# Kernel optimization log

Hardware: AMD Instinct MI355X
Metric: run time of the kernel (lower is better)

Reference implementation:

```python
import jax, jax.numpy as jnp
import numpy as np

EPS = 1e-5
NEG_SLOPE = 0.01

def layer_norm(x, w, b):
    m = jnp.mean(x, axis=-1, keepdims=True)
    v = jnp.var(x, axis=-1, keepdims=True)
    return (x - m) / jnp.sqrt(v + EPS) * w + b

def _lin_init(key, out_dim, in_dim):
    s = 1.0 / np.sqrt(in_dim)
    k1, k2 = jax.random.split(key)
    W = jax.random.uniform(k1, (out_dim, in_dim), jnp.float32, -s, s)
    b = jax.random.uniform(k2, (out_dim,), jnp.float32, -s, s)
    return W, b

def setup_inputs() -> dict:
    key = jax.random.key(0)
    ks = jax.random.split(key, 12)
    N_S = 100000; N_T = 100000; E = 2000000; H1 = 64; H2 = 32
    x_s = jax.random.normal(ks[0], (N_S, 2), jnp.float32)
    x_t = jax.random.normal(ks[1], (N_T, 2), jnp.float32)
    edge_index = jax.random.randint(ks[2], (2, E), 0, N_S, jnp.int32)
    edge_attr = jax.random.uniform(ks[3], (E,), jnp.float32)
    w0, b0 = _lin_init(ks[4], H1, 3)
    w1, b1 = _lin_init(ks[5], H1, H1)
    w2, b2 = _lin_init(ks[6], H1, H1)
    w3, b3 = _lin_init(ks[7], 1, H1)
    ln_w = jnp.ones((3, H1), jnp.float32)
    ln_b = jnp.zeros((3, H1), jnp.float32)
    fw1, fb1 = _lin_init(ks[8], H2, 4)
    fln_w = jnp.ones((H2,), jnp.float32)
    fln_b = jnp.zeros((H2,), jnp.float32)
    fw2, fb2 = _lin_init(ks[9], 1, H2)
    return dict(x_s=x_s, x_t=x_t, edge_index=edge_index, edge_attr=edge_attr,
                w0=w0, b0=b0, w1=w1, b1=b1, w2=w2, b2=b2, w3=w3, b3=b3,
                ln_w=ln_w, ln_b=ln_b, fw1=fw1, fb1=fb1, fln_w=fln_w, fln_b=fln_b,
                fw2=fw2, fb2=fb2)

def reference(x_s, x_t, edge_index, edge_attr, w0, b0, w1, b1, w2, b2, w3, b3,
              ln_w, ln_b, fw1, fb1, fln_w, fln_b, fw2, fb2):
    src = edge_index[0]
    dst = edge_index[1]
    x_s_d = x_s[src, 1][:, None]           # [E,1]
    x_s_c = x_t[dst, 1][:, None]           # [E,1]
    y = jnp.concatenate([x_s_d, x_s_c, edge_attr[:, None]], axis=1)  # [E,3]
    # MLP chain: Linear -> LeakyReLU -> (dropout eval: identity) -> LayerNorm
    for i, (W, b) in enumerate([(w0, b0), (w1, b1), (w2, b2)]):
        y = layer_norm(jax.nn.leaky_relu(y @ W.T + b, NEG_SLOPE), ln_w[i], ln_b[i])
    y = jax.nn.relu(y @ w3.T + b3)[:, 0]   # [E]
    # index_add scatter then re-gather
    y_sum_i = jax.ops.segment_sum(y, src, num_segments=x_s.shape[0])[src][:, None]
    y_sum_j = jax.ops.segment_sum(y, dst, num_segments=x_t.shape[0])[dst][:, None]
    coef = jnp.concatenate([x_s_d, y_sum_i, x_s_c, y_sum_j], axis=1)  # [E,4]
    coef = layer_norm(jax.nn.relu(coef @ fw1.T + fb1), fln_w, fln_b)
    coef = jax.nn.relu(coef @ fw2.T + fb2)[:, 0]
    return y * coef
```

## Files before the change

kernel.cpp:

```cpp
#include <hip/hip_runtime.h>

#define H2 32

#define SIG_F32  0x3F800000u
#define SIG_BF16 0x3F803F80u

typedef float v4f __attribute__((ext_vector_type(4)));
typedef short s8v __attribute__((ext_vector_type(8)));
typedef unsigned u4v __attribute__((ext_vector_type(4)));

__global__ void zero_f(float* __restrict__ p, int n) {
    int i = blockIdx.x * blockDim.x + threadIdx.x;
    if (i < n) p[i] = 0.0f;
}

template<bool BF16>
__device__ __forceinline__ float LD(const void* p, int i) {
    if (BF16) {
        unsigned int u = ((unsigned int)((const unsigned short*)p)[i]) << 16;
        return __uint_as_float(u);
    }
    return ((const float*)p)[i];
}

template<bool BF16>
__device__ __forceinline__ void ST(void* p, int i, float v) {
    if (BF16) {
        unsigned int u = __float_as_uint(v);
        unsigned int r = (u + 0x7FFFu + ((u >> 16) & 1u)) >> 16;
        ((unsigned short*)p)[i] = (unsigned short)r;
    } else {
        ((float*)p)[i] = v;
    }
}

__device__ __forceinline__ unsigned short bf16_rne(float x) {
    unsigned int u = __float_as_uint(x);
    return (unsigned short)((u + 0x7FFFu + ((u >> 16) & 1u)) >> 16);
}

__device__ __forceinline__ void split2(float x0, float x1,
                                       unsigned& hw, unsigned& lw) {
    unsigned h;
    asm("v_cvt_pk_bf16_f32 %0, %1, %2" : "=v"(h) : "v"(x0), "v"(x1));
    const float h0 = __uint_as_float(h << 16);
    const float h1 = __uint_as_float(h & 0xFFFF0000u);
    unsigned l;
    asm("v_cvt_pk_bf16_f32 %0, %1, %2" : "=v"(l) : "v"(x0 - h0), "v"(x1 - h1));
    hw = h; lw = l;
}

__device__ __align__(16) unsigned short g_A[2 * 2 * 4 * 2 * 512];
__device__ __align__(16) float g_S[2][64], g_C[2][64];
__device__ __align__(16) float g_l0[64 * 4];
__device__ __align__(16) float g_w3g[64];
__device__ float g_sc3[2];

template<bool BF16>
__device__ __forceinline__ void fold_body(
    const void* w0, const void* b0, const void* w1, const void* b1,
    const void* w2, const void* b2, const void* w3, const void* b3,
    const void* lnw, const void* lnb) {
    const int b = blockIdx.x;
    const int k = threadIdx.x;
    if (b < 128) {
        const int L = b >> 6, j = b & 63;
        const void* w  = L ? w2 : w1;
        const void* bb = L ? b2 : b1;
        const float wv = LD<BF16>(w, j * 64 + k);
        const float wt = wv * LD<BF16>(lnw, L * 64 + k);
        float s = wt;
        float c = wv * LD<BF16>(lnb, L * 64 + k);
        #pragma unroll
        for (int off = 1; off < 64; off <<= 1) {
            s += __shfl_xor(s, off);
            c += __shfl_xor(c, off);
        }
        if (k == 0) {
            g_S[L][j] = s;
            g_C[L][j] = c + LD<BF16>(bb, j);
        }
    } else {
        const int j = k;
        g_l0[4 * j + 0] = LD<BF16>(w0, 3 * j);
        g_l0[4 * j + 1] = LD<BF16>(w0, 3 * j + 1);
        g_l0[4 * j + 2] = LD<BF16>(w0, 3 * j + 2);
        g_l0[4 * j + 3] = LD<BF16>(b0, j);
        const float w3g = LD<BF16>(w3, j) * LD<BF16>(lnw, 128 + j);
        g_w3g[j] = w3g;
        float S = w3g;
        float C = LD<BF16>(w3, j) * LD<BF16>(lnb, 128 + j);
        #pragma unroll
        for (int off = 1; off < 64; off <<= 1) {
            S += __shfl_xor(S, off);
            C += __shfl_xor(C, off);
        }
        if (j == 0) { g_sc3[0] = S; g_sc3[1] = C + LD<BF16>(b3, 0); }
    }
}

__global__ void setup_fold(const void* __restrict__ w0, const void* __restrict__ b0,
                           const void* __restrict__ w1, const void* __restrict__ b1,
                           const void* __restrict__ w2, const void* __restrict__ b2,
                           const void* __restrict__ w3, const void* __restrict__ b3,
                           const void* __restrict__ lnw, const void* __restrict__ lnb) {
    const unsigned int sig = *(const unsigned int*)lnw;
    if (sig == SIG_BF16)
        fold_body<true>(w0, b0, w1, b1, w2, b2, w3, b3, lnw, lnb);
    else
        fold_body<false>(w0, b0, w1, b1, w2, b2, w3, b3, lnw, lnb);
}

template<bool BF16>
__device__ __forceinline__ void frag_body(const void* w1, const void* w2,
                                          const void* lnw) {
    const int b  = blockIdx.x;
    const int L  = b >> 3, jt = (b >> 1) & 3, ks = b & 1;
    const int l  = threadIdx.x, m = l & 15, g = l >> 4;
    const void* w = L ? w2 : w1;
    const int row = 16 * jt + m;
    const int blkH = ((L * 2 + 0) * 4 + jt) * 2 + ks;
    const int blkL = ((L * 2 + 1) * 4 + jt) * 2 + ks;
    #pragma unroll
    for (int i = 0; i < 8; ++i) {
        const int k = 32 * ks + 8 * g + i;
        const float x = LD<BF16>(w, row * 64 + k) * LD<BF16>(lnw, L * 64 + k);
        const unsigned short hi = bf16_rne(x);
        const float hif = __uint_as_float(((unsigned int)hi) << 16);
        const unsigned short lo = bf16_rne(x - hif);
        g_A[blkH * 512 + l * 8 + i] = hi;
        g_A[blkL * 512 + l * 8 + i] = lo;
    }
}

__global__ void setup_frag(const void* __restrict__ w1, const void* __restrict__ w2,
                           const void* __restrict__ lnw) {
    const unsigned int sig = *(const unsigned int*)lnw;
    if (sig == SIG_BF16) frag_body<true>(w1, w2, lnw);
    else                 frag_body<false>(w1, w2, lnw);
}

template<bool BF16>
__device__ __forceinline__ void edge_body(
    const void* xs, const void* xt, const int* ei, const void* ea,
    void* ystage, float* ssrc, float* sdst, int E, unsigned char* Hb) {

    const int tid = threadIdx.x;
    const int l   = tid & 63;
    const int wid = __builtin_amdgcn_readfirstlane(tid >> 6);
    unsigned char* Hw = Hb + wid * 8192;
    const int m16 = l & 15, g = l >> 4;

    const int tile = blockIdx.x * 4 + wid;
    const int e0 = tile * 32;
    if (e0 >= E) return;

    int srcA[2], dstA[2];
    float av[2], cv[2], wv[2];
    #pragma unroll
    for (int s = 0; s < 2; ++s) {
        int e = e0 + s * 16 + m16;
        int ec = e < E ? e : 0;
        srcA[s] = ei[ec]; dstA[s] = ei[E + ec];
        av[s] = LD<BF16>(xs, 2 * srcA[s] + 1);
        cv[s] = LD<BF16>(xt, 2 * dstA[s] + 1);
        wv[s] = LD<BF16>(ea, ec);
    }

    float m_[2], r_[2];

    s8v Bh[2][2], Bl[2][2];
    {
        float ps[2] = {0.f, 0.f}, ps2[2] = {0.f, 0.f};
        #pragma unroll
        for (int s = 0; s < 2; ++s) {
            #pragma unroll
            for (int ks = 0; ks < 2; ++ks) {
                u4v th, tl;
                #pragma unroll
                for (int q = 0; q < 4; ++q) {
                    const int f = 32 * ks + 8 * g + 2 * q;
                    const v4f qa = *(const v4f*)&g_l0[4 * f];
                    const v4f qb = *(const v4f*)&g_l0[4 * (f + 1)];
                    float x0 = qa.w + av[s] * qa.x + cv[s] * qa.y + wv[s] * qa.z;
                    float x1 = qb.w + av[s] * qb.x + cv[s] * qb.y + wv[s] * qb.z;
                    x0 = fmaxf(x0, 0.01f * x0);
                    x1 = fmaxf(x1, 0.01f * x1);
                    ps[s] += x0 + x1; ps2[s] += x0 * x0 + x1 * x1;
                    unsigned hw, lw;
                    split2(x0, x1, hw, lw);
                    th[q] = hw; tl[q] = lw;
                }
                Bh[s][ks] = __builtin_bit_cast(s8v, th);
                Bl[s][ks] = __builtin_bit_cast(s8v, tl);
            }
            float a0 = ps[s], a1 = ps2[s];
            a0 += __shfl_xor(a0, 16); a0 += __shfl_xor(a0, 32);
            a1 += __shfl_xor(a1, 16); a1 += __shfl_xor(a1, 32);
            m_[s] = a0 * (1.f / 64.f);
            r_[s] = rsqrtf(a1 * (1.f / 64.f) - m_[s] * m_[s] + 1e-5f);
        }
    }

    {
        float psA[2] = {0.f, 0.f}, ps2A[2] = {0.f, 0.f};
        #pragma unroll
        for (int jt = 0; jt < 4; ++jt) {
            const s8v Ah0 = *(const s8v*)(g_A + ((0 + jt) * 2 + 0) * 512 + l * 8);
            const s8v Ah1 = *(const s8v*)(g_A + ((0 + jt) * 2 + 1) * 512 + l * 8);
            const s8v Al0 = *(const s8v*)(g_A + ((4 + jt) * 2 + 0) * 512 + l * 8);
            const s8v Al1 = *(const s8v*)(g_A + ((4 + jt) * 2 + 1) * 512 + l * 8);
            const v4f Sv = *(const v4f*)&g_S[0][16 * jt + 4 * g];
            const v4f Cv = *(const v4f*)&g_C[0][16 * jt + 4 * g];
            #pragma unroll
            for (int s = 0; s < 2; ++s) {
                v4f a0 = {0.f, 0.f, 0.f, 0.f};
                v4f a1 = {0.f, 0.f, 0.f, 0.f};
                a0 = __builtin_amdgcn_mfma_f32_16x16x32_bf16(Ah0, Bh[s][0], a0, 0, 0, 0);
                a1 = __builtin_amdgcn_mfma_f32_16x16x32_bf16(Al0, Bh[s][0], a1, 0, 0, 0);
                a0 = __builtin_amdgcn_mfma_f32_16x16x32_bf16(Ah1, Bh[s][1], a0, 0, 0, 0);
                a1 = __builtin_amdgcn_mfma_f32_16x16x32_bf16(Al1, Bh[s][1], a1, 0, 0, 0);
                a0 = __builtin_amdgcn_mfma_f32_16x16x32_bf16(Ah0, Bl[s][0], a0, 0, 0, 0);
                a1 = __builtin_amdgcn_mfma_f32_16x16x32_bf16(Ah1, Bl[s][1], a1, 0, 0, 0);
                float x0 = r_[s] * ((a0[0] + a1[0]) - m_[s] * Sv[0]) + Cv[0];
                float x1 = r_[s] * ((a0[1] + a1[1]) - m_[s] * Sv[1]) + Cv[1];
                float x2 = r_[s] * ((a0[2] + a1[2]) - m_[s] * Sv[2]) + Cv[2];
                float x3 = r_[s] * ((a0[3] + a1[3]) - m_[s] * Sv[3]) + Cv[3];
                x0 = fmaxf(x0, 0.01f * x0); x1 = fmaxf(x1, 0.01f * x1);
                x2 = fmaxf(x2, 0.01f * x2); x3 = fmaxf(x3, 0.01f * x3);
                psA[s]  += x0 + x1 + x2 + x3;
                ps2A[s] += x0 * x0 + x1 * x1 + x2 * x2 + x3 * x3;
                unsigned hw0, lw0, hw1, lw1;
                split2(x0, x1, hw0, lw0);
                split2(x2, x3, hw1, lw1);
                const int el = s * 16 + m16;
                const unsigned sw = (unsigned)((el & 7) << 4);
                const unsigned off = (unsigned)el * 128
                                   + (((unsigned)(32 * jt + 8 * g)) ^ sw);
                uint2 ph; ph.x = hw0; ph.y = hw1;
                uint2 pl; pl.x = lw0; pl.y = lw1;
                *(uint2*)&Hw[off] = ph;
                *(uint2*)&Hw[off + 4096] = pl;
            }
        }
        #pragma unroll
        for (int s = 0; s < 2; ++s) {
            float ps = psA[s], ps2 = ps2A[s];
            ps  += __shfl_xor(ps, 16);  ps  += __shfl_xor(ps, 32);
            ps2 += __shfl_xor(ps2, 16); ps2 += __shfl_xor(ps2, 32);
            m_[s] = ps * (1.f / 64.f);
            r_[s] = rsqrtf(ps2 * (1.f / 64.f) - m_[s] * m_[s] + 1e-5f);
        }
    }

    float pd[2] = {0.f, 0.f};
    {
        #pragma unroll
        for (int s = 0; s < 2; ++s) {
            const int el = s * 16 + m16;
            const unsigned sw = (unsigned)((el & 7) << 4);
            #pragma unroll
            for (int ks = 0; ks < 2; ++ks) {
                const unsigned off = (unsigned)el * 128
                                   + (((unsigned)(16 * g + 64 * ks)) ^ sw);
                Bh[s][ks] = *(const s8v*)&Hw[off];
                Bl[s][ks] = *(const s8v*)&Hw[off + 4096];
            }
        }
        float psA[2] = {0.f, 0.f}, ps2A[2] = {0.f, 0.f};
        #pragma unroll
        for (int jt = 0; jt < 4; ++jt) {
            const s8v Ah0 = *(const s8v*)(g_A + ((8  + jt) * 2 + 0) * 512 + l * 8);
            const s8v Ah1 = *(const s8v*)(g_A + ((8  + jt) * 2 + 1) * 512 + l * 8);
            const s8v Al0 = *(const s8v*)(g_A + ((12 + jt) * 2 + 0) * 512 + l * 8);
            const s8v Al1 = *(const s8v*)(g_A + ((12 + jt) * 2 + 1) * 512 + l * 8);
            const v4f Sv = *(const v4f*)&g_S[1][16 * jt + 4 * g];
            const v4f Cv = *(const v4f*)&g_C[1][16 * jt + 4 * g];
            const v4f w3v = *(const v4f*)&g_w3g[16 * jt + 4 * g];
            #pragma unroll
            for (int s = 0; s < 2; ++s) {
                v4f a0 = {0.f, 0.f, 0.f, 0.f};
                v4f a1 = {0.f, 0.f, 0.f, 0.f};
                a0 = __builtin_amdgcn_mfma_f32_16x16x32_bf16(Ah0, Bh[s][0], a0, 0, 0, 0);
                a1 = __builtin_amdgcn_mfma_f32_16x16x32_bf16(Al0, Bh[s][0], a1, 0, 0, 0);
                a0 = __builtin_amdgcn_mfma_f32_16x16x32_bf16(Ah1, Bh[s][1], a0, 0, 0, 0);
                a1 = __builtin_amdgcn_mfma_f32_16x16x32_bf16(Al1, Bh[s][1], a1, 0, 0, 0);
                a0 = __builtin_amdgcn_mfma_f32_16x16x32_bf16(Ah0, Bl[s][0], a0, 0, 0, 0);
                a1 = __builtin_amdgcn_mfma_f32_16x16x32_bf16(Ah1, Bl[s][1], a1, 0, 0, 0);
                #pragma unroll
                for (int r = 0; r < 4; ++r) {
                    float x = r_[s] * ((a0[r] + a1[r]) - m_[s] * Sv[r]) + Cv[r];
                    x = fmaxf(x, 0.01f * x);
                    psA[s] += x; ps2A[s] += x * x;
                    pd[s] += x * w3v[r];
                }
            }
        }
        #pragma unroll
        for (int s = 0; s < 2; ++s) {
            float ps = psA[s], ps2 = ps2A[s];
            ps  += __shfl_xor(ps, 16);  ps  += __shfl_xor(ps, 32);
            ps2 += __shfl_xor(ps2, 16); ps2 += __shfl_xor(ps2, 32);
            m_[s] = ps * (1.f / 64.f);
            r_[s] = rsqrtf(ps2 * (1.f / 64.f) - m_[s] * m_[s] + 1e-5f);
        }
    }

    #pragma unroll
    for (int s = 0; s < 2; ++s) {
        float d = pd[s];
        d += __shfl_xor(d, 16); d += __shfl_xor(d, 32);
        float t = r_[s] * (d - m_[s] * g_sc3[0]) + g_sc3[1];
        const float yv = fmaxf(t, 0.f);
        if (g == 0) {
            int e = e0 + s * 16 + m16;
            if (e < E) {
                ST<BF16>(ystage, e, yv);
                atomicAdd(&ssrc[srcA[s]], yv);
                atomicAdd(&sdst[dstA[s]], yv);
            }
        }
    }
}

__global__ __launch_bounds__(256, 2)
void edge_mfma(const void* __restrict__ xs, const void* __restrict__ xt,
               const int* __restrict__ ei, const void* __restrict__ ea,
               const void* __restrict__ lnw,
               void* __restrict__ ystage,
               float* __restrict__ ssrc, float* __restrict__ sdst, int E) {
    __shared__ __align__(16) unsigned char lds[4][8192];
    const unsigned int sig = *(const unsigned int*)lnw;
    if (sig == SIG_BF16)
        edge_body<true>(xs, xt, ei, ea, ystage, ssrc, sdst, E, &lds[0][0]);
    else
        edge_body<false>(xs, xt, ei, ea, ystage, ssrc, sdst, E, &lds[0][0]);
}

template<bool BF16>
__device__ __forceinline__ void coef_body(
    const void* xs, const void* xt, const int* ei,
    const void* fw1, const void* fb1, const void* flnw, const void* flnb,
    const void* fw2, const void* fb2,
    const float* ssrc, const float* sdst, void* out, int E) {
    int e = blockIdx.x * blockDim.x + threadIdx.x;
    if (e >= E) return;
    const int src = ei[e], dst = ei[E + e];
    const float c0 = LD<BF16>(xs, 2 * src + 1);
    const float c2 = LD<BF16>(xt, 2 * dst + 1);
    const float c1 = ssrc[src];
    const float c3 = sdst[dst];
    float h[H2];
    float sum = 0.f, sum2 = 0.f;
    #pragma unroll
    for (int j = 0; j < H2; ++j) {
        float t = LD<BF16>(fb1, j) + c0 * LD<BF16>(fw1, 4 * j) + c1 * LD<BF16>(fw1, 4 * j + 1)
                + c2 * LD<BF16>(fw1, 4 * j + 2) + c3 * LD<BF16>(fw1, 4 * j + 3);
        t = (t > 0.f) ? t : 0.f;
        h[j] = t; sum += t; sum2 += t * t;
    }
    const float m = sum * (1.f / H2);
    const float r = rsqrtf(sum2 * (1.f / H2) - m * m + 1e-5f);
    float t = LD<BF16>(fb2, 0);
    #pragma unroll
    for (int j = 0; j < H2; ++j)
        t += ((h[j] - m) * r * LD<BF16>(flnw, j) + LD<BF16>(flnb, j)) * LD<BF16>(fw2, j);
    const float coef = (t > 0.f) ? t : 0.f;
    const float yv = LD<BF16>(out, e);
    ST<BF16>(out, e, yv * coef);
}

__global__ __launch_bounds__(256)
void coef_stage(const void* __restrict__ xs, const void* __restrict__ xt,
                const int* __restrict__ ei,
                const void* __restrict__ fw1, const void* __restrict__ fb1,
                const void* __restrict__ flnw, const void* __restrict__ flnb,
                const void* __restrict__ fw2, const void* __restrict__ fb2,
                const void* __restrict__ lnw,
                const float* __restrict__ ssrc, const float* __restrict__ sdst,
                void* __restrict__ out, int E) {
    const unsigned int sig = *(const unsigned int*)lnw;
    if (sig == SIG_BF16)
        coef_body<true>(xs, xt, ei, fw1, fb1, flnw, flnb, fw2, fb2, ssrc, sdst, out, E);
    else
        coef_body<false>(xs, xt, ei, fw1, fb1, flnw, flnb, fw2, fb2, ssrc, sdst, out, E);
}

extern "C" void kernel_launch(void* const* d_in, const int* in_sizes, int n_in,
                              void* d_out, int out_size, void* d_ws, size_t ws_size,
                              hipStream_t stream) {
    const void* xs = d_in[0];
    const void* xt = d_in[1];
    const int*  ei = (const int*)d_in[2];
    const void* ea = d_in[3];
    const int NS = in_sizes[0] / 2;
    const int NT = in_sizes[1] / 2;
    const int E  = in_sizes[3];

    float* ws   = (float*)d_ws;
    float* ssrc = ws;
    float* sdst = ws + NS;

    const int nz = NS + NT;
    const int gE = (E + 255) / 256;
    zero_f<<<(nz + 255) / 256, 256, 0, stream>>>(ws, nz);

    setup_fold<<<129, 64, 0, stream>>>(
        d_in[4], d_in[5], d_in[6], d_in[7], d_in[8], d_in[9],
        d_in[10], d_in[11], d_in[12], d_in[13]);
    setup_frag<<<16, 64, 0, stream>>>(d_in[6], d_in[8], d_in[12]);

    const int tiles  = (E + 31) / 32;
    const int blocks = (tiles + 3) / 4;
    edge_mfma<<<blocks, 256, 0, stream>>>(
        xs, xt, ei, ea, d_in[12], d_out, ssrc, sdst, E);

    coef_stage<<<gE, 256, 0, stream>>>(
        xs, xt, ei, d_in[14], d_in[15], d_in[16], d_in[17], d_in[18], d_in[19],
        d_in[12], ssrc, sdst, d_out, E);
}
```

Measured before the change: 374.1 us.

## Make edge MFMA kernel persistent with software-prefetched gathers for next tile

The edge kernel becomes a grid-stride persistent loop capped at 1024 blocks. Each wave processes several 32-edge tiles and issues the index and feature gathers for its next tile while the current tile's MFMA layers run, so gather latency is hidden behind compute. The costs are extra live registers for the prefetched data, which may hurt occupancy, and fewer waves in flight to hide latency in other ways.

```diff
diff --git a/kernel.cpp b/kernel.cpp
--- a/kernel.cpp
+++ b/kernel.cpp
@@ -140,6 +140,11 @@
     else                 frag_body<false>(w1, w2, lnw);
 }
 
+struct EdgeData {
+    int   src[2], dst[2];
+    float av[2], cv[2], wv[2];
+};
+
 template<bool BF16>
 __device__ __forceinline__ void edge_body(
     const void* xs, const void* xt, const int* ei, const void* ea,
@@ -151,175 +156,200 @@
     unsigned char* Hw = Hb + wid * 8192;
     const int m16 = l & 15, g = l >> 4;
 
-    const int tile = blockIdx.x * 4 + wid;
-    const int e0 = tile * 32;
-    if (e0 >= E) return;
-
-    int srcA[2], dstA[2];
-    float av[2], cv[2], wv[2];
-    #pragma unroll
-    for (int s = 0; s < 2; ++s) {
-        int e = e0 + s * 16 + m16;
-        int ec = e < E ? e : 0;
-        srcA[s] = ei[ec]; dstA[s] = ei[E + ec];
-        av[s] = LD<BF16>(xs, 2 * srcA[s] + 1);
-        cv[s] = LD<BF16>(xt, 2 * dstA[s] + 1);
-        wv[s] = LD<BF16>(ea, ec);
-    }
-
-    float m_[2], r_[2];
-
-    s8v Bh[2][2], Bl[2][2];
+    const int ntiles = (E + 31) >> 5;
+    const int nwaves = gridDim.x * 4;
+    int t = blockIdx.x * 4 + wid;
+    if (t >= ntiles) return;
+
+    EdgeData ed;
     {
-        float ps[2] = {0.f, 0.f}, ps2[2] = {0.f, 0.f};
+        const int e0 = t << 5;
         #pragma unroll
         for (int s = 0; s < 2; ++s) {
-            #pragma unroll
-            for (int ks = 0; ks < 2; ++ks) {
-                u4v th, tl;
+            int e = e0 + s * 16 + m16;
+            int ec = e < E ? e : 0;
+            ed.src[s] = ei[ec]; ed.dst[s] = ei[E + ec];
+            ed.av[s] = LD<BF16>(xs, 2 * ed.src[s] + 1);
+            ed.cv[s] = LD<BF16>(xt, 2 * ed.dst[s] + 1);
+            ed.wv[s] = LD<BF16>(ea, ec);
+        }
+    }
+
+    for (; t < ntiles; t += nwaves) {
+        const int e0 = t << 5;
+        float m_[2], r_[2];
+        s8v Bh[2][2], Bl[2][2];
+
+        {
+            float ps[2] = {0.f, 0.f}, ps2[2] = {0.f, 0.f};
+            #pragma unroll
+            for (int s = 0; s < 2; ++s) {
                 #pragma unroll
-                for (int q = 0; q < 4; ++q) {
-                    const int f = 32 * ks + 8 * g + 2 * q;
-                    const v4f qa = *(const v4f*)&g_l0[4 * f];
-                    const v4f qb = *(const v4f*)&g_l0[4 * (f + 1)];
-                    float x0 = qa.w + av[s] * qa.x + cv[s] * qa.y + wv[s] * qa.z;
-                    float x1 = qb.w + av[s] * qb.x + cv[s] * qb.y + wv[s] * qb.z;
-                    x0 = fmaxf(x0, 0.01f * x0);
-                    x1 = fmaxf(x1, 0.01f * x1);
-                    ps[s] += x0 + x1; ps2[s] += x0 * x0 + x1 * x1;
-                    unsigned hw, lw;
-                    split2(x0, x1, hw, lw);
-                    th[q] = hw; tl[q] = lw;
+                for (int ks = 0; ks < 2; ++ks) {
+                    u4v th, tl;
+                    #pragma unroll
+                    for (int q = 0; q < 4; ++q) {
+                        const int f = 32 * ks + 8 * g + 2 * q;
+                        const v4f qa = *(const v4f*)&g_l0[4 * f];
+                        const v4f qb = *(const v4f*)&g_l0[4 * (f + 1)];
+                        float x0 = qa.w + ed.av[s] * qa.x + ed.cv[s] * qa.y + ed.wv[s] * qa.z;
+                        float x1 = qb.w + ed.av[s] * qb.x + ed.cv[s] * qb.y + ed.wv[s] * qb.z;
+                        x0 = fmaxf(x0, 0.01f * x0);
+                        x1 = fmaxf(x1, 0.01f * x1);
+                        ps[s] += x0 + x1; ps2[s] += x0 * x0 + x1 * x1;
+                        unsigned hw, lw;
+                        split2(x0, x1, hw, lw);
+                        th[q] = hw; tl[q] = lw;
+                    }
+                    Bh[s][ks] = __builtin_bit_cast(s8v, th);
+                    Bl[s][ks] = __builtin_bit_cast(s8v, tl);
                 }
-                Bh[s][ks] = __builtin_bit_cast(s8v, th);
-                Bl[s][ks] = __builtin_bit_cast(s8v, tl);
-            }
-            float a0 = ps[s], a1 = ps2[s];
-            a0 += __shfl_xor(a0, 16); a0 += __shfl_xor(a0, 32);
-            a1 += __shfl_xor(a1, 16); a1 += __shfl_xor(a1, 32);
-            m_[s] = a0 * (1.f / 64.f);
-            r_[s] = rsqrtf(a1 * (1.f / 64.f) - m_[s] * m_[s] + 1e-5f);
-        }
-    }
-
-    {
-        float psA[2] = {0.f, 0.f}, ps2A[2] = {0.f, 0.f};
-        #pragma unroll
-        for (int jt = 0; jt < 4; ++jt) {
-            const s8v Ah0 = *(const s8v*)(g_A + ((0 + jt) * 2 + 0) * 512 + l * 8);
-            const s8v Ah1 = *(const s8v*)(g_A + ((0 + jt) * 2 + 1) * 512 + l * 8);
-            const s8v Al0 = *(const s8v*)(g_A + ((4 + jt) * 2 + 0) * 512 + l * 8);
-            const s8v Al1 = *(const s8v*)(g_A + ((4 + jt) * 2 + 1) * 512 + l * 8);
-            const v4f Sv = *(const v4f*)&g_S[0][16 * jt + 4 * g];
-            const v4f Cv = *(const v4f*)&g_C[0][16 * jt + 4 * g];
+                float a0 = ps[s], a1 = ps2[s];
+                a0 += __shfl_xor(a0, 16); a0 += __shfl_xor(a0, 32);
+                a1 += __shfl_xor(a1, 16); a1 += __shfl_xor(a1, 32);
+                m_[s] = a0 * (1.f / 64.f);
+                r_[s] = rsqrtf(a1 * (1.f / 64.f) - m_[s] * m_[s] + 1e-5f);
+            }
+        }
+
+        const int csrc0 = ed.src[0], csrc1 = ed.src[1];
+        const int cdst0 = ed.dst[0], cdst1 = ed.dst[1];
+        const int tn = t + nwaves;
+        if (tn < ntiles) {
+            const int ne0 = tn << 5;
             #pragma unroll
             for (int s = 0; s < 2; ++s) {
-                v4f a0 = {0.f, 0.f, 0.f, 0.f};
-                v4f a1 = {0.f, 0.f, 0.f, 0.f};
-                a0 = __builtin_amdgcn_mfma_f32_16x16x32_bf16(Ah0, Bh[s][0], a0, 0, 0, 0);
-                a1 = __builtin_amdgcn_mfma_f32_16x16x32_bf16(Al0, Bh[s][0], a1, 0, 0, 0);
-                a0 = __builtin_amdgcn_mfma_f32_16x16x32_bf16(Ah1, Bh[s][1], a0, 0, 0, 0);
-                a1 = __builtin_amdgcn_mfma_f32_16x16x32_bf16(Al1, Bh[s][1], a1, 0, 0, 0);
-                a0 = __builtin_amdgcn_mfma_f32_16x16x32_bf16(Ah0, Bl[s][0], a0, 0, 0, 0);
-                a1 = __builtin_amdgcn_mfma_f32_16x16x32_bf16(Ah1, Bl[s][1], a1, 0, 0, 0);
-                float x0 = r_[s] * ((a0[0] + a1[0]) - m_[s] * Sv[0]) + Cv[0];
-                float x1 = r_[s] * ((a0[1] + a1[1]) - m_[s] * Sv[1]) + Cv[1];
-                float x2 = r_[s] * ((a0[2] + a1[2]) - m_[s] * Sv[2]) + Cv[2];
-                float x3 = r_[s] * ((a0[3] + a1[3]) - m_[s] * Sv[3]) + Cv[3];
-                x0 = fmaxf(x0, 0.01f * x0); x1 = fmaxf(x1, 0.01f * x1);
-                x2 = fmaxf(x2, 0.01f * x2); x3 = fmaxf(x3, 0.01f * x3);
-                psA[s]  += x0 + x1 + x2 + x3;
-                ps2A[s] += x0 * x0 + x1 * x1 + x2 * x2 + x3 * x3;
-                unsigned hw0, lw0, hw1, lw1;
-                split2(x0, x1, hw0, lw0);
-                split2(x2, x3, hw1, lw1);
+                int e = ne0 + s * 16 + m16;
+                int ec = e < E ? e : 0;
+                ed.src[s] = ei[ec]; ed.dst[s] = ei[E + ec];
+                ed.av[s] = LD<BF16>(xs, 2 * ed.src[s] + 1);
+                ed.cv[s] = LD<BF16>(xt, 2 * ed.dst[s] + 1);
+                ed.wv[s] = LD<BF16>(ea, ec);
+            }
+        }
+
+        {
+            float psA[2] = {0.f, 0.f}, ps2A[2] = {0.f, 0.f};
+            #pragma unroll
+            for (int jt = 0; jt < 4; ++jt) {
+                const s8v Ah0 = *(const s8v*)(g_A + ((0 + jt) * 2 + 0) * 512 + l * 8);
+                const s8v Ah1 = *(const s8v*)(g_A + ((0 + jt) * 2 + 1) * 512 + l * 8);
+                const s8v Al0 = *(const s8v*)(g_A + ((4 + jt) * 2 + 0) * 512 + l * 8);
+                const s8v Al1 = *(const s8v*)(g_A + ((4 + jt) * 2 + 1) * 512 + l * 8);
+                const v4f Sv = *(const v4f*)&g_S[0][16 * jt + 4 * g];
+                const v4f Cv = *(const v4f*)&g_C[0][16 * jt + 4 * g];
+                #pragma unroll
+                for (int s = 0; s < 2; ++s) {
+                    v4f a0 = {0.f, 0.f, 0.f, 0.f};
+                    v4f a1 = {0.f, 0.f, 0.f, 0.f};
+                    a0 = __builtin_amdgcn_mfma_f32_16x16x32_bf16(Ah0, Bh[s][0], a0, 0, 0, 0);
+                    a1 = __builtin_amdgcn_mfma_f32_16x16x32_bf16(Al0, Bh[s][0], a1, 0, 0, 0);
+                    a0 = __builtin_amdgcn_mfma_f32_16x16x32_bf16(Ah1, Bh[s][1], a0, 0, 0, 0);
+                    a1 = __builtin_amdgcn_mfma_f32_16x16x32_bf16(Al1, Bh[s][1], a1, 0, 0, 0);
+                    a0 = __builtin_amdgcn_mfma_f32_16x16x32_bf16(Ah0, Bl[s][0], a0, 0, 0, 0);
+                    a1 = __builtin_amdgcn_mfma_f32_16x16x32_bf16(Ah1, Bl[s][1], a1, 0, 0, 0);
+                    float x0 = r_[s] * ((a0[0] + a1[0]) - m_[s] * Sv[0]) + Cv[0];
+                    float x1 = r_[s] * ((a0[1] + a1[1]) - m_[s] * Sv[1]) + Cv[1];
+                    float x2 = r_[s] * ((a0[2] + a1[2]) - m_[s] * Sv[2]) + Cv[2];
+                    float x3 = r_[s] * ((a0[3] + a1[3]) - m_[s] * Sv[3]) + Cv[3];
+                    x0 = fmaxf(x0, 0.01f * x0); x1 = fmaxf(x1, 0.01f * x1);
+                    x2 = fmaxf(x2, 0.01f * x2); x3 = fmaxf(x3, 0.01f * x3);
+                    psA[s]  += x0 + x1 + x2 + x3;
+                    ps2A[s] += x0 * x0 + x1 * x1 + x2 * x2 + x3 * x3;
+                    unsigned hw0, lw0, hw1, lw1;
+                    split2(x0, x1, hw0, lw0);
+                    split2(x2, x3, hw1, lw1);
+                    const int el = s * 16 + m16;
+                    const unsigned sw = (unsigned)((el & 7) << 4);
+                    const unsigned off = (unsigned)el * 128
+                                       + (((unsigned)(32 * jt + 8 * g)) ^ sw);
+                    uint2 ph; ph.x = hw0; ph.y = hw1;
+                    uint2 pl; pl.x = lw0; pl.y = lw1;
+                    *(uint2*)&Hw[off] = ph;
+                    *(uint2*)&Hw[off + 4096] = pl;
+                }
+            }
+            #pragma unroll
+            for (int s = 0; s < 2; ++s) {
+                float ps = psA[s], ps2 = ps2A[s];
+                ps  += __shfl_xor(ps, 16);  ps  += __shfl_xor(ps, 32);
+                ps2 += __shfl_xor(ps2, 16); ps2 += __shfl_xor(ps2, 32);
+                m_[s] = ps * (1.f / 64.f);
+                r_[s] = rsqrtf(ps2 * (1.f / 64.f) - m_[s] * m_[s] + 1e-5f);
+            }
+        }
+
+        float pd[2] = {0.f, 0.f};
+        {
+            #pragma unroll
+            for (int s = 0; s < 2; ++s) {
                 const int el = s * 16 + m16;
                 const unsigned sw = (unsigned)((el & 7) << 4);
-                const unsigned off = (unsigned)el * 128
-                                   + (((unsigned)(32 * jt + 8 * g)) ^ sw);
-                uint2 ph; ph.x = hw0; ph.y = hw1;
-                uint2 pl; pl.x = lw0; pl.y = lw1;
-                *(uint2*)&Hw[off] = ph;
-                *(uint2*)&Hw[off + 4096] = pl;
-            }
-        }
+                #pragma unroll
+                for (int ks = 0; ks < 2; ++ks) {
+                    const unsigned off = (unsigned)el * 128
+                                       + (((unsigned)(16 * g + 64 * ks)) ^ sw);
+                    Bh[s][ks] = *(const s8v*)&Hw[off];
+                    Bl[s][ks] = *(const s8v*)&Hw[off + 4096];
+                }
+            }
+            float psA[2] = {0.f, 0.f}, ps2A[2] = {0.f, 0.f};
+            #pragma unroll
+            for (int jt = 0; jt < 4; ++jt) {
+                const s8v Ah0 = *(const s8v*)(g_A + ((8  + jt) * 2 + 0) * 512 + l * 8);
+                const s8v Ah1 = *(const s8v*)(g_A + ((8  + jt) * 2 + 1) * 512 + l * 8);
+                const s8v Al0 = *(const s8v*)(g_A + ((12 + jt) * 2 + 0) * 512 + l * 8);
+                const s8v Al1 = *(const s8v*)(g_A + ((12 + jt) * 2 + 1) * 512 + l * 8);
+                const v4f Sv = *(const v4f*)&g_S[1][16 * jt + 4 * g];
+                const v4f Cv = *(const v4f*)&g_C[1][16 * jt + 4 * g];
+                const v4f w3v = *(const v4f*)&g_w3g[16 * jt + 4 * g];
+                #pragma unroll
+                for (int s = 0; s < 2; ++s) {
+                    v4f a0 = {0.f, 0.f, 0.f, 0.f};
+                    v4f a1 = {0.f, 0.f, 0.f, 0.f};
+                    a0 = __builtin_amdgcn_mfma_f32_16x16x32_bf16(Ah0, Bh[s][0], a0, 0, 0, 0);
+                    a1 = __builtin_amdgcn_mfma_f32_16x16x32_bf16(Al0, Bh[s][0], a1, 0, 0, 0);
+                    a0 = __builtin_amdgcn_mfma_f32_16x16x32_bf16(Ah1, Bh[s][1], a0, 0, 0, 0);
+                    a1 = __builtin_amdgcn_mfma_f32_16x16x32_bf16(Al1, Bh[s][1], a1, 0, 0, 0);
+                    a0 = __builtin_amdgcn_mfma_f32_16x16x32_bf16(Ah0, Bl[s][0], a0, 0, 0, 0);
+                    a1 = __builtin_amdgcn_mfma_f32_16x16x32_bf16(Ah1, Bl[s][1], a1, 0, 0, 0);
+                    #pragma unroll
+                    for (int r = 0; r < 4; ++r) {
+                        float x = r_[s] * ((a0[r] + a1[r]) - m_[s] * Sv[r]) + Cv[r];
+                        x = fmaxf(x, 0.01f * x);
+                        psA[s] += x; ps2A[s] += x * x;
+                        pd[s] += x * w3v[r];
+                    }
+                }
+            }
+            #pragma unroll
+            for (int s = 0; s < 2; ++s) {
+                float ps = psA[s], ps2 = ps2A[s];
+                ps  += __shfl_xor(ps, 16);  ps  += __shfl_xor(ps, 32);
+                ps2 += __shfl_xor(ps2, 16); ps2 += __shfl_xor(ps2, 32);
+                m_[s] = ps * (1.f / 64.f);
+                r_[s] = rsqrtf(ps2 * (1.f / 64.f) - m_[s] * m_[s] + 1e-5f);
+            }
+        }
+
         #pragma unroll
         for (int s = 0; s < 2; ++s) {
-            float ps = psA[s], ps2 = ps2A[s];
-            ps  += __shfl_xor(ps, 16);  ps  += __shfl_xor(ps, 32);
-            ps2 += __shfl_xor(ps2, 16); ps2 += __shfl_xor(ps2, 32);
-            m_[s] = ps * (1.f / 64.f);
-            r_[s] = rsqrtf(ps2 * (1.f / 64.f) - m_[s] * m_[s] + 1e-5f);
-        }
-    }
-
-    float pd[2] = {0.f, 0.f};
-    {
-        #pragma unroll
-        for (int s = 0; s < 2; ++s) {
-            const int el = s * 16 + m16;
-            const unsigned sw = (unsigned)((el & 7) << 4);
-            #pragma unroll
-            for (int ks = 0; ks < 2; ++ks) {
-                const unsigned off = (unsigned)el * 128
-                                   + (((unsigned)(16 * g + 64 * ks)) ^ sw);
-                Bh[s][ks] = *(const s8v*)&Hw[off];
-                Bl[s][ks] = *(const s8v*)&Hw[off + 4096];
-            }
-        }
-        float psA[2] = {0.f, 0.f}, ps2A[2] = {0.f, 0.f};
-        #pragma unroll
-        for (int jt = 0; jt < 4; ++jt) {
-            const s8v Ah0 = *(const s8v*)(g_A + ((8  + jt) * 2 + 0) * 512 + l * 8);
-            const s8v Ah1 = *(const s8v*)(g_A + ((8  + jt) * 2 + 1) * 512 + l * 8);
-            const s8v Al0 = *(const s8v*)(g_A + ((12 + jt) * 2 + 0) * 512 + l * 8);
-            const s8v Al1 = *(const s8v*)(g_A + ((12 + jt) * 2 + 1) * 512 + l * 8);
-            const v4f Sv = *(const v4f*)&g_S[1][16 * jt + 4 * g];
-            const v4f Cv = *(const v4f*)&g_C[1][16 * jt + 4 * g];
-            const v4f w3v = *(const v4f*)&g_w3g[16 * jt + 4 * g];
-            #pragma unroll
-            for (int s = 0; s < 2; ++s) {
-                v4f a0 = {0.f, 0.f, 0.f, 0.f};
-                v4f a1 = {0.f, 0.f, 0.f, 0.f};
-                a0 = __builtin_amdgcn_mfma_f32_16x16x32_bf16(Ah0, Bh[s][0], a0, 0, 0, 0);
-                a1 = __builtin_amdgcn_mfma_f32_16x16x32_bf16(Al0, Bh[s][0], a1, 0, 0, 0);
-                a0 = __builtin_amdgcn_mfma_f32_16x16x32_bf16(Ah1, Bh[s][1], a0, 0, 0, 0);
-                a1 = __builtin_amdgcn_mfma_f32_16x16x32_bf16(Al1, Bh[s][1], a1, 0, 0, 0);
-                a0 = __builtin_amdgcn_mfma_f32_16x16x32_bf16(Ah0, Bl[s][0], a0, 0, 0, 0);
-                a1 = __builtin_amdgcn_mfma_f32_16x16x32_bf16(Ah1, Bl[s][1], a1, 0, 0, 0);
-                #pragma unroll
-                for (int r = 0; r < 4; ++r) {
-                    float x = r_[s] * ((a0[r] + a1[r]) - m_[s] * Sv[r]) + Cv[r];
-                    x = fmaxf(x, 0.01f * x);
-                    psA[s] += x; ps2A[s] += x * x;
-                    pd[s] += x * w3v[r];
+            float d = pd[s];
+            d += __shfl_xor(d, 16); d += __shfl_xor(d, 32);
+            float tt = r_[s] * (d - m_[s] * g_sc3[0]) + g_sc3[1];
+            const float yv = fmaxf(tt, 0.f);
+            if (g == 0) {
+                int e = e0 + s * 16 + m16;
+                if (e < E) {
+                    ST<BF16>(ystage, e, yv);
+                    atomicAdd(&ssrc[s ? csrc1 : csrc0], yv);
+                    atomicAdd(&sdst[s ? cdst1 : cdst0], yv);
                 }
             }
         }
-        #pragma unroll
-        for (int s = 0; s < 2; ++s) {
-            float ps = psA[s], ps2 = ps2A[s];
-            ps  += __shfl_xor(ps, 16);  ps  += __shfl_xor(ps, 32);
-            ps2 += __shfl_xor(ps2, 16); ps2 += __shfl_xor(ps2, 32);
-            m_[s] = ps * (1.f / 64.f);
-            r_[s] = rsqrtf(ps2 * (1.f / 64.f) - m_[s] * m_[s] + 1e-5f);
-        }
-    }
-
-    #pragma unroll
-    for (int s = 0; s < 2; ++s) {
-        float d = pd[s];
-        d += __shfl_xor(d, 16); d += __shfl_xor(d, 32);
-        float t = r_[s] * (d - m_[s] * g_sc3[0]) + g_sc3[1];
-        const float yv = fmaxf(t, 0.f);
-        if (g == 0) {
-            int e = e0 + s * 16 + m16;
-            if (e < E) {
-                ST<BF16>(ystage, e, yv);
-                atomicAdd(&ssrc[srcA[s]], yv);
-                atomicAdd(&sdst[dstA[s]], yv);
-            }
-        }
+
+        asm volatile("" ::: "memory");
+        __builtin_amdgcn_sched_barrier(0);
     }
 }
 
@@ -411,7 +441,8 @@
     setup_frag<<<16, 64, 0, stream>>>(d_in[6], d_in[8], d_in[12]);
 
     const int tiles  = (E + 31) / 32;
-    const int blocks = (tiles + 3) / 4;
+    int blocks = (tiles + 3) / 4;
+    if (blocks > 1024) blocks = 1024;
     edge_mfma<<<blocks, 256, 0, stream>>>(
         xs, xt, ei, ea, d_in[12], d_out, ssrc, sdst, E);
 
```

New measurement: 392.0 us. 1.05x slower.
